# Performance work log

Measured on AMD Instinct MI355X. Metric: run time of the kernel, lower is better.

Reference implementation:

```python
import jax, jax.numpy as jnp
import numpy as np

HIDDEN = 768
MLP_RATIO = 4
HID_F = HIDDEN * MLP_RATIO          # 3072
NUM_EXPERTS = 6
PART = 192                           # part_features
SHARED = HIDDEN - PART               # 576
B, S = 32, 1024


def setup_inputs() -> dict:
    key = jax.random.key(0)
    ks = jax.random.split(key, 8)
    hidden_state = jax.random.normal(ks[0], (B, S, HIDDEN), dtype=jnp.float32)
    indices = jax.random.randint(ks[1], (B,), 0, NUM_EXPERTS, dtype=jnp.int64)
    sc1 = 1.0 / np.sqrt(HIDDEN)
    sc2 = 1.0 / np.sqrt(HID_F)
    W1 = jax.random.normal(ks[2], (HIDDEN, HID_F), dtype=jnp.float32) * sc1
    b1 = jax.random.normal(ks[3], (HID_F,), dtype=jnp.float32) * sc1
    W2 = jax.random.normal(ks[4], (HID_F, SHARED), dtype=jnp.float32) * sc2
    b2 = jax.random.normal(ks[5], (SHARED,), dtype=jnp.float32) * sc2
    We = jax.random.normal(ks[6], (NUM_EXPERTS, HID_F, PART), dtype=jnp.float32) * sc2
    be = jax.random.normal(ks[7], (NUM_EXPERTS, PART), dtype=jnp.float32) * sc2
    return {"hidden_state": hidden_state, "indices": indices,
            "W1": W1, "b1": b1, "W2": W2, "b2": b2, "We": We, "be": be}


def reference(hidden_state, indices, W1, b1, W2, b2, We, be):
    # fc1 + exact GELU (torch ACT2FN['gelu'])
    h = jnp.einsum('bsd,df->bsf', hidden_state, W1) + b1          # [B,S,HID_F]
    h = jax.nn.gelu(h, approximate=False)
    # shared branch
    shared = jnp.einsum('bsf,fo->bso', h, W2) + b2                # [B,S,SHARED]
    # expert branch: indices select exactly one expert per batch element,
    # so the masked sum over all experts equals gathering the routed expert.
    Wsel = We[indices]                                            # [B,HID_F,PART]
    bsel = be[indices]                                            # [B,PART]
    expert = jnp.einsum('bsf,bfp->bsp', h, Wsel) + bsel[:, None, :]
    return jnp.concatenate([shared, expert], axis=-1)             # [B,S,HIDDEN]
```

## Files before the change

kernel.cpp:

```cpp
#include <hip/hip_runtime.h>
#include <hip/hip_bf16.h>
#include <cstdint>
#include <cstddef>

#define HIDDEN   768
#define HID_F    3072
#define PART     192
#define SHARED_F 576
#define NEXP     6
#define BATCH    32
#define SEQ      1024
#define M_TOK    (BATCH * SEQ)

typedef __bf16 bf16;
typedef __attribute__((ext_vector_type(8))) __bf16 bf16x8;
typedef __attribute__((ext_vector_type(4))) __bf16 bf16x4;
typedef __attribute__((ext_vector_type(4))) float  f32x4;

__device__ __forceinline__ void gl2lds16(const void* g, void* l) {
    __builtin_amdgcn_global_load_lds(
        (const __attribute__((address_space(1))) void*)g,
        (__attribute__((address_space(3))) void*)l,
        16, 0, 0);
}

__device__ __forceinline__ float gelu_fast(float x) {
    float xs = x * 0.70710678118654752f;
    float ax = __builtin_fabsf(xs);
    float t  = __builtin_amdgcn_rcpf(1.0f + 0.3275911f * ax);
    float p  = t * (0.254829592f +
               t * (-0.284496736f +
               t * (1.421413741f +
               t * (-1.453152027f +
               t * 1.061405429f))));
    float e  = __expf(-xs * xs);
    float er = 1.0f - p * e;
    er = (xs < 0.0f) ? -er : er;
    return 0.5f * x * (1.0f + er);
}

__global__ __launch_bounds__(256) void cvt_f32_bf16(
        const float4* __restrict__ src, bf16x4* __restrict__ dst, int n4) {
    int i      = blockIdx.x * 256 + threadIdx.x;
    int stride = gridDim.x * 256;
    for (; i < n4; i += stride) {
        float4 v = src[i];
        bf16x4 o = { (__bf16)v.x, (__bf16)v.y, (__bf16)v.z, (__bf16)v.w };
        dst[i] = o;
    }
}

__global__ __launch_bounds__(256) void transpose_cvt(
        const float* __restrict__ src, bf16* __restrict__ dst, int K, int N) {
    __shared__ float t[32][33];
    const int n0 = blockIdx.x * 32, k0 = blockIdx.y * 32;
    const int tx = threadIdx.x & 31, ty = threadIdx.x >> 5;
#pragma unroll
    for (int p = 0; p < 4; ++p) {
        int r = ty + p * 8;
        t[r][tx] = src[(size_t)(k0 + r) * N + n0 + tx];
    }
    __syncthreads();
#pragma unroll
    for (int p = 0; p < 4; ++p) {
        int rn = ty + p * 8;
        dst[(size_t)(n0 + rn) * K + k0 + tx] = (bf16)t[tx][rn];
    }
}

__global__ __launch_bounds__(256) void build_wcat(
        const float* __restrict__ W2, const float* __restrict__ We,
        bf16* __restrict__ Wcat) {
    __shared__ float t[32][33];
    const int e  = blockIdx.z;
    const int n0 = blockIdx.x * 32;
    const int k0 = blockIdx.y * 32;
    const int tx = threadIdx.x & 31, ty = threadIdx.x >> 5;
    const float* src;
    int ld, c;
    if (n0 < SHARED_F) { src = W2; ld = SHARED_F; c = n0 + tx; }
    else { src = We + (size_t)e * HID_F * PART; ld = PART; c = n0 + tx - SHARED_F; }
#pragma unroll
    for (int p = 0; p < 4; ++p) {
        int r = ty + p * 8;
        t[r][tx] = src[(size_t)(k0 + r) * ld + c];
    }
    __syncthreads();
    bf16* dst = Wcat + (size_t)e * HIDDEN * HID_F;
#pragma unroll
    for (int p = 0; p < 4; ++p) {
        int rn = ty + p * 8;
        dst[(size_t)(n0 + rn) * HID_F + k0 + tx] = (bf16)t[tx][rn];
    }
}


__global__ __launch_bounds__(256) void fc1_gelu(
        const bf16* __restrict__ A,
        const bf16* __restrict__ Bt,
        const float* __restrict__ b1,
        bf16* __restrict__ H) {
    __shared__ alignas(16) bf16 As[128 * 32];
    __shared__ alignas(16) bf16 Bs[128 * 32];
    const int tid  = threadIdx.x;
    const int wave = tid >> 6, lane = tid & 63;
    const int wm = wave >> 1, wn = wave & 1;
    const int lrow = lane & 15, lk8 = lane >> 4;

    const int L   = blockIdx.x;
    const int xcd = L & 7;
    const int j   = L >> 3;
    const int jm  = j / 24;
    const int mt  = xcd * 32 + jm;
    const int nt  = j - jm * 24;
    const int m0 = mt * 128;
    const int n0 = nt * 128;

    const int srow   = lane >> 2;
    const int schunk = (((lane & 3) ^ ((lane >> 3) & 3))) * 8;
    const int rchunk = ((lk8 ^ ((lrow >> 1) & 3))) * 8;

    const bf16* gA0 = A  + (size_t)(m0 + wave * 32 + srow) * HIDDEN + schunk;
    const bf16* gA1 = gA0 + 16 * HIDDEN;
    const bf16* gB0 = Bt + (size_t)(n0 + wave * 32 + srow) * HIDDEN + schunk;
    const bf16* gB1 = gB0 + 16 * HIDDEN;
    bf16* lA0 = As + (wave * 32) * 32;
    bf16* lA1 = lA0 + 16 * 32;
    bf16* lB0 = Bs + (wave * 32) * 32;
    bf16* lB1 = lB0 + 16 * 32;

    f32x4 acc[4][4] = {};
    for (int k0 = 0; k0 < HIDDEN; k0 += 32) {
        gl2lds16(gA0, lA0); gl2lds16(gA1, lA1);
        gl2lds16(gB0, lB0); gl2lds16(gB1, lB1);
        gA0 += 32; gA1 += 32; gB0 += 32; gB1 += 32;
        __syncthreads();
        bf16x8 af[4], bfr[4];
#pragma unroll
        for (int mi = 0; mi < 4; ++mi)
            af[mi] = *(const bf16x8*)(As + (wm * 64 + mi * 16 + lrow) * 32 + rchunk);
#pragma unroll
        for (int ni = 0; ni < 4; ++ni)
            bfr[ni] = *(const bf16x8*)(Bs + (wn * 64 + ni * 16 + lrow) * 32 + rchunk);
#pragma unroll
        for (int mi = 0; mi < 4; ++mi)
#pragma unroll
            for (int ni = 0; ni < 4; ++ni)
                acc[mi][ni] = __builtin_amdgcn_mfma_f32_16x16x32_bf16(
                    af[mi], bfr[ni], acc[mi][ni], 0, 0, 0);
        __syncthreads();
    }
#pragma unroll
    for (int mi = 0; mi < 4; ++mi) {
#pragma unroll
        for (int ni = 0; ni < 4; ++ni) {
            int col = n0 + wn * 64 + ni * 16 + lrow;
            float bias = b1[col];
#pragma unroll
            for (int r = 0; r < 4; ++r) {
                int row = m0 + wm * 64 + mi * 16 + lk8 * 4 + r;
                float v = acc[mi][ni][r] + bias;
                H[(size_t)row * HID_F + col] = (bf16)gelu_fast(v);
            }
        }
    }
}

__global__ __launch_bounds__(256) void fc2_moe(
        const bf16* __restrict__ H,
        const bf16* __restrict__ Wcat,
        const float* __restrict__ b2,
        const float* __restrict__ be,
        const int*  __restrict__ idx,
        float* __restrict__ Out) {
    __shared__ alignas(16) bf16 As[128 * 32];
    __shared__ alignas(16) bf16 Bs[128 * 32];
    const int tid  = threadIdx.x;
    const int wave = tid >> 6, lane = tid & 63;
    const int wm = wave >> 1, wn = wave & 1;
    const int lrow = lane & 15, lk8 = lane >> 4;

    const int L   = blockIdx.x;
    const int xcd = L & 7;
    const int j   = L >> 3;
    const int jm  = j / 6;
    const int mt  = xcd * 32 + jm;
    const int nt  = j - jm * 6;
    const int m0 = mt * 128;
    const int n0 = nt * 128;

    int e = idx[mt >> 3];
    e = e < 0 ? 0 : (e > NEXP - 1 ? NEXP - 1 : e);
    const bf16* Bt = Wcat + (size_t)e * HIDDEN * HID_F;
    const int srow   = lane >> 2;
    const int schunk = (((lane & 3) ^ ((lane >> 3) & 3))) * 8;
    const int rchunk = ((lk8 ^ ((lrow >> 1) & 3))) * 8;

    const bf16* gA0 = H  + (size_t)(m0 + wave * 32 + srow) * HID_F + schunk;
    const bf16* gA1 = gA0 + 16 * HID_F;
    const bf16* gB0 = Bt + (size_t)(n0 + wave * 32 + srow) * HID_F + schunk;
    const bf16* gB1 = gB0 + 16 * HID_F;
    bf16* lA0 = As + (wave * 32) * 32;
    bf16* lA1 = lA0 + 16 * 32;
    bf16* lB0 = Bs + (wave * 32) * 32;
    bf16* lB1 = lB0 + 16 * 32;

    f32x4 acc[4][4] = {};
    for (int k0 = 0; k0 < HID_F; k0 += 32) {
        gl2lds16(gA0, lA0); gl2lds16(gA1, lA1);
        gl2lds16(gB0, lB0); gl2lds16(gB1, lB1);
        gA0 += 32; gA1 += 32; gB0 += 32; gB1 += 32;
        __syncthreads();
        bf16x8 af[4], bfr[4];
#pragma unroll
        for (int mi = 0; mi < 4; ++mi)
            af[mi] = *(const bf16x8*)(As + (wm * 64 + mi * 16 + lrow) * 32 + rchunk);
#pragma unroll
        for (int ni = 0; ni < 4; ++ni)
            bfr[ni] = *(const bf16x8*)(Bs + (wn * 64 + ni * 16 + lrow) * 32 + rchunk);
#pragma unroll
        for (int mi = 0; mi < 4; ++mi)
#pragma unroll
            for (int ni = 0; ni < 4; ++ni)
                acc[mi][ni] = __builtin_amdgcn_mfma_f32_16x16x32_bf16(
                    af[mi], bfr[ni], acc[mi][ni], 0, 0, 0);
        __syncthreads();
    }
#pragma unroll
    for (int mi = 0; mi < 4; ++mi) {
#pragma unroll
        for (int ni = 0; ni < 4; ++ni) {
            int col = n0 + wn * 64 + ni * 16 + lrow;
            float bias = (col < SHARED_F) ? b2[col] : be[e * PART + col - SHARED_F];
#pragma unroll
            for (int r = 0; r < 4; ++r) {
                int row = m0 + wm * 64 + mi * 16 + lk8 * 4 + r;
                Out[(size_t)row * HIDDEN + col] = acc[mi][ni][r] + bias;
            }
        }
    }
}

extern "C" void kernel_launch(void* const* d_in, const int* in_sizes, int n_in,
                              void* d_out, int out_size, void* d_ws, size_t ws_size,
                              hipStream_t stream) {
    const float* hidden = (const float*)d_in[0];
    const int*   idx    = (const int*)d_in[1];
    const float* W1     = (const float*)d_in[2];
    const float* b1     = (const float*)d_in[3];
    const float* W2     = (const float*)d_in[4];
    const float* b2     = (const float*)d_in[5];
    const float* We     = (const float*)d_in[6];
    const float* be     = (const float*)d_in[7];
    float* out = (float*)d_out;

    char* ws = (char*)d_ws;
    bf16* hb   = (bf16*)(ws);
    bf16* h    = (bf16*)(ws + 50331648);
    bf16* W1t  = (bf16*)(ws + 251658240);
    bf16* Wcat = (bf16*)(ws + 256376832);

    cvt_f32_bf16<<<4096, 256, 0, stream>>>(
        (const float4*)hidden, (bf16x4*)hb, (M_TOK * HIDDEN) / 4);
    transpose_cvt<<<dim3(HID_F / 32, HIDDEN / 32), 256, 0, stream>>>(
        W1, W1t, HIDDEN, HID_F);
    build_wcat<<<dim3(HIDDEN / 32, HID_F / 32, NEXP), 256, 0, stream>>>(
        W2, We, Wcat);

    fc1_gelu<<<(HID_F / 128) * (M_TOK / 128), 256, 0, stream>>>(hb, W1t, b1, h);

    fc2_moe<<<(HIDDEN / 128) * (M_TOK / 128), 256, 0, stream>>>(
        h, Wcat, b2, be, idx, out);
}
```

Before: 618.0 us.

## Double-buffer LDS tiles in fc1 and fc2 GEMM main loops

Both GEMM kernels now allocate two LDS buffers per operand, load the first K-tile before the loop, and issue the next tile's global-to-LDS loads before computing on the current one. The goal is to overlap global memory latency with the MFMA work instead of waiting on each load right before compute. In exchange, LDS per block doubles to 32 KB, which may reduce how many blocks fit on a CU. Overlap also depends on the barrier at the end of each iteration not forcing the prefetch to finish too early.

```diff
diff --git a/kernel.cpp b/kernel.cpp
--- a/kernel.cpp
+++ b/kernel.cpp
@@ -11,6 +11,8 @@
 #define BATCH    32
 #define SEQ      1024
 #define M_TOK    (BATCH * SEQ)
+
+#define BUFE (128 * 32)
 
 typedef __bf16 bf16;
 typedef __attribute__((ext_vector_type(8))) __bf16 bf16x8;
@@ -100,8 +102,8 @@
         const bf16* __restrict__ Bt,
         const float* __restrict__ b1,
         bf16* __restrict__ H) {
-    __shared__ alignas(16) bf16 As[128 * 32];
-    __shared__ alignas(16) bf16 Bs[128 * 32];
+    __shared__ alignas(16) bf16 As[2 * BUFE];
+    __shared__ alignas(16) bf16 Bs[2 * BUFE];
     const int tid  = threadIdx.x;
     const int wave = tid >> 6, lane = tid & 63;
     const int wm = wave >> 1, wn = wave & 1;
@@ -129,19 +131,30 @@
     bf16* lB0 = Bs + (wave * 32) * 32;
     bf16* lB1 = lB0 + 16 * 32;
 
+    gl2lds16(gA0, lA0); gl2lds16(gA1, lA1);
+    gl2lds16(gB0, lB0); gl2lds16(gB1, lB1);
+    gA0 += 32; gA1 += 32; gB0 += 32; gB1 += 32;
+    __syncthreads();
+
     f32x4 acc[4][4] = {};
-    for (int k0 = 0; k0 < HIDDEN; k0 += 32) {
-        gl2lds16(gA0, lA0); gl2lds16(gA1, lA1);
-        gl2lds16(gB0, lB0); gl2lds16(gB1, lB1);
-        gA0 += 32; gA1 += 32; gB0 += 32; gB1 += 32;
-        __syncthreads();
+    const int NIT = HIDDEN / 32;
+    for (int it = 0; it < NIT; ++it) {
+        const int cur = it & 1;
+        if (it + 1 < NIT) {
+            const int off = (cur ^ 1) * BUFE;
+            gl2lds16(gA0, lA0 + off); gl2lds16(gA1, lA1 + off);
+            gl2lds16(gB0, lB0 + off); gl2lds16(gB1, lB1 + off);
+            gA0 += 32; gA1 += 32; gB0 += 32; gB1 += 32;
+        }
+        const bf16* Ab = As + cur * BUFE;
+        const bf16* Bb = Bs + cur * BUFE;
         bf16x8 af[4], bfr[4];
 #pragma unroll
         for (int mi = 0; mi < 4; ++mi)
-            af[mi] = *(const bf16x8*)(As + (wm * 64 + mi * 16 + lrow) * 32 + rchunk);
+            af[mi] = *(const bf16x8*)(Ab + (wm * 64 + mi * 16 + lrow) * 32 + rchunk);
 #pragma unroll
         for (int ni = 0; ni < 4; ++ni)
-            bfr[ni] = *(const bf16x8*)(Bs + (wn * 64 + ni * 16 + lrow) * 32 + rchunk);
+            bfr[ni] = *(const bf16x8*)(Bb + (wn * 64 + ni * 16 + lrow) * 32 + rchunk);
 #pragma unroll
         for (int mi = 0; mi < 4; ++mi)
 #pragma unroll
@@ -173,8 +186,8 @@
         const float* __restrict__ be,
         const int*  __restrict__ idx,
         float* __restrict__ Out) {
-    __shared__ alignas(16) bf16 As[128 * 32];
-    __shared__ alignas(16) bf16 Bs[128 * 32];
+    __shared__ alignas(16) bf16 As[2 * BUFE];
+    __shared__ alignas(16) bf16 Bs[2 * BUFE];
     const int tid  = threadIdx.x;
     const int wave = tid >> 6, lane = tid & 63;
     const int wm = wave >> 1, wn = wave & 1;
@@ -191,33 +204,45 @@
 
     int e = idx[mt >> 3];
     e = e < 0 ? 0 : (e > NEXP - 1 ? NEXP - 1 : e);
-    const bf16* Bt = Wcat + (size_t)e * HIDDEN * HID_F;
+    const bf16* Btp = Wcat + (size_t)e * HIDDEN * HID_F;
+
     const int srow   = lane >> 2;
     const int schunk = (((lane & 3) ^ ((lane >> 3) & 3))) * 8;
     const int rchunk = ((lk8 ^ ((lrow >> 1) & 3))) * 8;
 
-    const bf16* gA0 = H  + (size_t)(m0 + wave * 32 + srow) * HID_F + schunk;
+    const bf16* gA0 = H   + (size_t)(m0 + wave * 32 + srow) * HID_F + schunk;
     const bf16* gA1 = gA0 + 16 * HID_F;
-    const bf16* gB0 = Bt + (size_t)(n0 + wave * 32 + srow) * HID_F + schunk;
+    const bf16* gB0 = Btp + (size_t)(n0 + wave * 32 + srow) * HID_F + schunk;
     const bf16* gB1 = gB0 + 16 * HID_F;
     bf16* lA0 = As + (wave * 32) * 32;
     bf16* lA1 = lA0 + 16 * 32;
     bf16* lB0 = Bs + (wave * 32) * 32;
     bf16* lB1 = lB0 + 16 * 32;
 
+    gl2lds16(gA0, lA0); gl2lds16(gA1, lA1);
+    gl2lds16(gB0, lB0); gl2lds16(gB1, lB1);
+    gA0 += 32; gA1 += 32; gB0 += 32; gB1 += 32;
+    __syncthreads();
+
     f32x4 acc[4][4] = {};
-    for (int k0 = 0; k0 < HID_F; k0 += 32) {
-        gl2lds16(gA0, lA0); gl2lds16(gA1, lA1);
-        gl2lds16(gB0, lB0); gl2lds16(gB1, lB1);
-        gA0 += 32; gA1 += 32; gB0 += 32; gB1 += 32;
-        __syncthreads();
+    const int NIT = HID_F / 32;
+    for (int it = 0; it < NIT; ++it) {
+        const int cur = it & 1;
+        if (it + 1 < NIT) {
+            const int off = (cur ^ 1) * BUFE;
+            gl2lds16(gA0, lA0 + off); gl2lds16(gA1, lA1 + off);
+            gl2lds16(gB0, lB0 + off); gl2lds16(gB1, lB1 + off);
+            gA0 += 32; gA1 += 32; gB0 += 32; gB1 += 32;
+        }
+        const bf16* Ab = As + cur * BUFE;
+        const bf16* Bb = Bs + cur * BUFE;
         bf16x8 af[4], bfr[4];
 #pragma unroll
         for (int mi = 0; mi < 4; ++mi)
-            af[mi] = *(const bf16x8*)(As + (wm * 64 + mi * 16 + lrow) * 32 + rchunk);
+            af[mi] = *(const bf16x8*)(Ab + (wm * 64 + mi * 16 + lrow) * 32 + rchunk);
 #pragma unroll
         for (int ni = 0; ni < 4; ++ni)
-            bfr[ni] = *(const bf16x8*)(Bs + (wn * 64 + ni * 16 + lrow) * 32 + rchunk);
+            bfr[ni] = *(const bf16x8*)(Bb + (wn * 64 + ni * 16 + lrow) * 32 + rchunk);
 #pragma unroll
         for (int mi = 0; mi < 4; ++mi)
 #pragma unroll
```

After: 670.6 us. 1.09x slower.
